# Kernel optimization log

Measured on AMD Instinct MI355X. Metric: run time of the kernel, lower is better.

Reference implementation:

```python
import jax, jax.numpy as jnp
import numpy as np

N_QUBITS = 12
BATCH = 2048
N_CLASSES = 10


def build_tape(n):
    # 2 layers of: RX on all wires (id 0), RY (id 1), RZ (id 2), then a CRX ring
    # (id 4 forward in layer 0, id 5 reversed in layer 1). 96 gates total for n=12.
    tape = []
    for layer in range(2):
        for i in range(n):
            tape.append(("rx", (i,)))
        for i in range(n):
            tape.append(("ry", (i,)))
        for i in range(n):
            tape.append(("rz", (i,)))
        order = range(n) if layer == 0 else range(n - 1, -1, -1)
        for i in order:
            tape.append(("crx", (i, (i + 1) % n)))
    return tape


def rx_mat(t):
    c = jnp.cos(t / 2).astype(jnp.complex64)
    s = jnp.sin(t / 2).astype(jnp.complex64)
    return jnp.stack([jnp.stack([c, -1j * s]), jnp.stack([-1j * s, c])])


def ry_mat(t):
    c = jnp.cos(t / 2).astype(jnp.complex64)
    s = jnp.sin(t / 2).astype(jnp.complex64)
    return jnp.stack([jnp.stack([c, -s]), jnp.stack([s, c])])


def rz_mat(t):
    em = jnp.exp(-1j * t.astype(jnp.complex64) / 2)
    ep = jnp.exp(1j * t.astype(jnp.complex64) / 2)
    z = jnp.zeros((), jnp.complex64)
    return jnp.stack([jnp.stack([em, z]), jnp.stack([z, ep])])


def apply_1q(psi, U, w):
    # psi: [B] + [2]*n, gate on wire w (axis 1+w)
    psi = jnp.moveaxis(psi, 1 + w, -1)
    psi = psi @ U.T
    return jnp.moveaxis(psi, -1, 1 + w)


def apply_crx(psi, theta, c, t):
    a_c, a_t = 1 + c, 1 + t
    psi = jnp.moveaxis(psi, a_c, 1)  # control -> axis 1
    if a_t < a_c:
        a_t += 1
    psi = jnp.moveaxis(psi, a_t, -1)  # target -> last axis
    U = rx_mat(theta)
    p1 = psi[:, 1] @ U.T  # apply RX only on control=1 branch
    psi = jnp.stack([psi[:, 0], p1], axis=1)
    psi = jnp.moveaxis(psi, -1, a_t)
    return jnp.moveaxis(psi, 1, a_c)


def expvals(psi, n):
    # <X_i>, <Y_i>, <Z_i> for each qubit; returns [B, 3n] ordered X..Y..Z (PL order)
    xs, ys, zs = [], [], []
    for i in range(n):
        p = jnp.moveaxis(psi, 1 + i, -1).reshape(psi.shape[0], -1, 2)
        z = jnp.sum(jnp.abs(p[..., 0]) ** 2 - jnp.abs(p[..., 1]) ** 2, axis=1)
        cross = jnp.sum(jnp.conj(p[..., 0]) * p[..., 1], axis=1)
        xs.append(2.0 * jnp.real(cross))
        ys.append(2.0 * jnp.imag(cross))
        zs.append(jnp.real(z))
    return jnp.stack(xs + ys + zs, axis=1).astype(jnp.float32)


def setup_inputs() -> dict:
    key = jax.random.key(0)
    k0, k1, k2 = jax.random.split(key, 3)
    sv = jax.random.normal(k0, (BATCH, 2 ** N_QUBITS), dtype=jnp.float32)
    sv = sv / jnp.linalg.norm(sv, axis=1, keepdims=True)  # valid quantum states
    n_gates = len(build_tape(N_QUBITS))
    angles = jax.random.normal(k1, (n_gates,), dtype=jnp.float32)
    W = jax.random.normal(k2, (N_CLASSES, 3 * N_QUBITS), dtype=jnp.float32) * 0.1
    b = jnp.zeros((N_CLASSES,), jnp.float32)
    return {"state_vectors": sv, "angles": angles, "W": W, "b": b}


def reference(state_vectors, angles, W, b):
    tape = build_tape(N_QUBITS)
    psi = state_vectors.astype(jnp.complex64).reshape((-1,) + (2,) * N_QUBITS)
    for g, (kind, wires) in enumerate(tape):
        th = angles[g]
        if kind == "rx":
            psi = apply_1q(psi, rx_mat(th), wires[0])
        elif kind == "ry":
            psi = apply_1q(psi, ry_mat(th), wires[0])
        elif kind == "rz":
            psi = apply_1q(psi, rz_mat(th), wires[0])
        else:
            psi = apply_crx(psi, th, wires[0], wires[1])
    feats = expvals(psi, N_QUBITS)  # [B, 3*n_qubits]
    return feats @ W.T + b
```

## Files before the change

kernel.cpp:

```cpp
#include <hip/hip_runtime.h>

#define DIM 4096
using F2 = float2;


__device__ __forceinline__ int swz(int i)            { return i ^ (i >> 6); }
__device__ __forceinline__ int addrA(int r, int t)   { return (r << 8) | t; }
__device__ __forceinline__ int addrB(int r, int t)   { return ((t >> 5) << 9) | (r << 5) | (t & 31); }
__device__ __forceinline__ int addrC(int r, int t)   { return ((t >> 2) << 6) | (r << 2) | (t & 3); }
__device__ __forceinline__ int addrD(int r, int t)   { return ((r >> 3) << 11) | (t << 3) | (r & 7); }

__device__ __forceinline__ F2 pk_mul_bl(F2 a, F2 u) {
    F2 d;
    asm("v_pk_mul_f32 %0, %1, %2 op_sel:[0,0] op_sel_hi:[1,0]"
        : "=v"(d) : "v"(a), "v"(u));
    return d;
}
__device__ __forceinline__ void pk_cross(F2& d, F2 a, F2 u) {
    asm("v_pk_fma_f32 %0, %1, %2, %0 op_sel:[1,1,0] op_sel_hi:[0,1,1] neg_lo:[1,0,0]"
        : "+v"(d) : "v"(a), "v"(u));
}
__device__ __forceinline__ void pk_fma_bl(F2& d, F2 a, F2 u) {
    asm("v_pk_fma_f32 %0, %1, %2, %0 op_sel:[0,0,0] op_sel_hi:[1,0,1]"
        : "+v"(d) : "v"(a), "v"(u));
}
__device__ __forceinline__ void pk_swapneg(F2& d, F2 a, F2 cs) {
    asm("v_pk_fma_f32 %0, %1, %2, %0 op_sel:[1,1,0] op_sel_hi:[0,1,1] neg_hi:[1,0,0]"
        : "+v"(d) : "v"(a), "v"(cs));
}
__device__ __forceinline__ void pk_fma(F2& d, F2 a, F2 b) {
    asm("v_pk_fma_f32 %0, %1, %2, %0" : "+v"(d) : "v"(a), "v"(b));
}
__device__ __forceinline__ void pk_imacc(F2& d, F2 a0, F2 a1) {
    asm("v_pk_fma_f32 %0, %1, %2, %0 op_sel:[0,1,0] op_sel_hi:[1,0,1] neg_hi:[1,0,0]"
        : "+v"(d) : "v"(a0), "v"(a1));
}
__device__ __forceinline__ F2 pk_cmul(F2 u, F2 a) {
    F2 d = pk_mul_bl(a, u);
    pk_cross(d, a, u);
    return d;
}
__device__ __forceinline__ void pk_cfma(F2& d, F2 u, F2 a) {
    pk_fma_bl(d, a, u);
    pk_cross(d, a, u);
}

__device__ __forceinline__ void build_u(float tx, float ty, float tz, float* u) {
    float sx = sinf(0.5f*tx), cx = cosf(0.5f*tx);
    float sy = sinf(0.5f*ty), cy = cosf(0.5f*ty);
    float sz = sinf(0.5f*tz), cz = cosf(0.5f*tz);
    float A00r = cy*cx, A00i =  sy*sx;
    float A01r = -sy*cx, A01i = -cy*sx;
    float A10r =  sy*cx, A10i = -cy*sx;
    float A11r =  cy*cx, A11i = -sy*sx;
    u[0] = cz*A00r + sz*A00i;  u[1] = cz*A00i - sz*A00r;
    u[2] = cz*A01r + sz*A01i;  u[3] = cz*A01i - sz*A01r;
    u[4] = cz*A10r - sz*A10i;  u[5] = cz*A10i + sz*A10r;
    u[6] = cz*A11r - sz*A11i;  u[7] = cz*A11i + sz*A11r;
}

__global__ void prep_kernel(const float* __restrict__ ang, float* __restrict__ coef) {
    int t = threadIdx.x;
    if (t < 24) {
        int l = t / 12, q = t % 12;
        float u[8];
        build_u(ang[48*l + q], ang[48*l + 12 + q], ang[48*l + 24 + q], u);
#pragma unroll
        for (int j = 0; j < 8; ++j) coef[t * 8 + j] = u[j];
    } else if (t < 48) {
        int g = t - 24;
        float th = 0.5f * ang[g < 12 ? 36 + g : 72 + g];
        coef[192 + g * 2]     = cosf(th);
        coef[192 + g * 2 + 1] = sinf(th);
    }
}

template<int M>
__device__ __forceinline__ void g1q(F2* amp, const float* __restrict__ u) {
    F2 u00 = {u[0], u[1]}, u01 = {u[2], u[3]};
    F2 u10 = {u[4], u[5]}, u11 = {u[6], u[7]};
#pragma unroll
    for (int r0 = 0; r0 < 16; ++r0) {
        if (r0 & M) continue;
        const int r1 = r0 + M;
        F2 a0 = amp[r0], a1 = amp[r1];
        F2 n0 = pk_cmul(u00, a0); pk_cfma(n0, u01, a1);
        F2 n1 = pk_cmul(u10, a0); pk_cfma(n1, u11, a1);
        amp[r0] = n0; amp[r1] = n1;
    }
}

template<int MC, int MT>
__device__ __forceinline__ void crx(F2* amp, F2 cs) {
#pragma unroll
    for (int r0 = 0; r0 < 16; ++r0) {
        if (!(r0 & MC) || (r0 & MT)) continue;
        const int r1 = r0 + MT;
        F2 a0 = amp[r0], a1 = amp[r1];
        F2 n0 = pk_mul_bl(a0, cs); pk_swapneg(n0, a1, cs);
        F2 n1 = pk_mul_bl(a1, cs); pk_swapneg(n1, a0, cs);
        amp[r0] = n0; amp[r1] = n1;
    }
}

template<int M>
__device__ __forceinline__ void expv(const F2* amp, int q, int lane,
                                     float& fx, float& fy, float& fz) {
    F2 zp = {0.f, 0.f}, zm = {0.f, 0.f}, xp = {0.f, 0.f}, ip = {0.f, 0.f};
#pragma unroll
    for (int r0 = 0; r0 < 16; ++r0) {
        if (r0 & M) continue;
        const int r1 = r0 + M;
        F2 a0 = amp[r0], a1 = amp[r1];
        pk_fma(zp, a0, a0);
        pk_fma(zm, a1, a1);
        pk_fma(xp, a0, a1);
        pk_imacc(ip, a0, a1);
    }
    float zz = (zp.x + zp.y) - (zm.x + zm.y);
    float xr = 2.f * (xp.x + xp.y);
    float xi = 2.f * (ip.x + ip.y);
#pragma unroll
    for (int off = 32; off; off >>= 1) {
        xr += __shfl_xor(xr, off);
        xi += __shfl_xor(xi, off);
        zz += __shfl_xor(zz, off);
    }
    if (lane == q) { fx = xr; fy = xi; fz = zz; }
}

#define XPOSE(CUR, NXT) \
  { _Pragma("unroll") for (int r = 0; r < 16; ++r) psi[swz(CUR(r, t))] = amp[r]; \
    __syncthreads(); \
    _Pragma("unroll") for (int r = 0; r < 16; ++r) amp[r] = psi[swz(NXT(r, t))]; \
    __syncthreads(); }

#define U0(q, M)        g1q<M>(amp, cf + (q) * 8)
#define U1(q, M)        g1q<M>(amp, cf + (12 + (q)) * 8)
#define CR0(c, MC, MT)  crx<MC, MT>(amp, F2{cf[192 + (c)*2], cf[192 + (c)*2 + 1]})
#define CR1(c, MC, MT)  crx<MC, MT>(amp, F2{cf[192 + (23-(c))*2], cf[192 + (23-(c))*2 + 1]})
#define EXPV(q, M)      expv<M>(amp, q, lane, fx, fy, fz)

__global__ __launch_bounds__(256, 1)
void qsim_kernel(const float* __restrict__ sv,
                 const float* __restrict__ cf,
                 const float* __restrict__ W,
                 const float* __restrict__ bvec,
                 float* __restrict__ out)
{
    __shared__ F2 psi[DIM];
    const int t = threadIdx.x;
    const int b = blockIdx.x;
    const int lane = t & 63, w = t >> 6;

    F2 amp[16];
    const float* svb = sv + (size_t)b * DIM;
#pragma unroll
    for (int r = 0; r < 16; ++r)
        amp[r] = make_float2(svb[(r << 8) | t], 0.f);

    float fx = 0.f, fy = 0.f, fz = 0.f;

    U0(0, 8); U0(1, 4); U0(2, 2); U0(3, 1);
    CR0(0, 8, 4); CR0(1, 4, 2); CR0(2, 2, 1);
    XPOSE(addrA, addrB);

    U0(4, 4); U0(5, 2); U0(6, 1);
    CR0(3, 8, 4); CR0(4, 4, 2); CR0(5, 2, 1);
    XPOSE(addrB, addrC);

    U0(7, 4); U0(8, 2); U0(9, 1);
    CR0(6, 8, 4); CR0(7, 4, 2); CR0(8, 2, 1);
    XPOSE(addrC, addrD);

    U0(10, 2); U0(11, 1);
    CR0(9, 4, 2); CR0(10, 2, 1); CR0(11, 1, 8);
    U1(9, 4); U1(10, 2); U1(11, 1); U1(0, 8);
    CR1(11, 1, 8); CR1(10, 2, 1); CR1(9, 4, 2);
    EXPV(10, 2); EXPV(11, 1);
    XPOSE(addrD, addrC);

    U1(6, 8); U1(7, 4); U1(8, 2);
    CR1(8, 2, 1); CR1(7, 4, 2); CR1(6, 8, 4);
    EXPV(9, 1); EXPV(8, 2); EXPV(7, 4);
    XPOSE(addrC, addrB);

    U1(3, 8); U1(4, 4); U1(5, 2);
    CR1(5, 2, 1); CR1(4, 4, 2); CR1(3, 8, 4);
    EXPV(6, 1); EXPV(5, 2); EXPV(4, 4);
    XPOSE(addrB, addrA);

    U1(1, 4); U1(2, 2);
    CR1(2, 2, 1); CR1(1, 4, 2); CR1(0, 8, 4);
    EXPV(0, 8); EXPV(1, 4); EXPV(2, 2); EXPV(3, 1);

    float* fbuf = (float*)psi;
    if (lane < 12) {
        fbuf[w * 36 + lane]      = fx;
        fbuf[w * 36 + 12 + lane] = fy;
        fbuf[w * 36 + 24 + lane] = fz;
    }
    __syncthreads();
    if (t < 10) {
        float a = bvec[t];
#pragma unroll
        for (int f = 0; f < 36; ++f)
            a += W[t * 36 + f] * (fbuf[f] + fbuf[36 + f] + fbuf[72 + f] + fbuf[108 + f]);
        out[(size_t)b * 10 + t] = a;
    }
}

extern "C" void kernel_launch(void* const* d_in, const int* in_sizes, int n_in,
                              void* d_out, int out_size, void* d_ws, size_t ws_size,
                              hipStream_t stream) {
    const float* sv     = (const float*)d_in[0];
    const float* angles = (const float*)d_in[1];
    const float* W      = (const float*)d_in[2];
    const float* bvec   = (const float*)d_in[3];
    float* out  = (float*)d_out;
    float* coef = (float*)d_ws;
    int batch = in_sizes[0] / DIM;
    prep_kernel<<<1, 64, 0, stream>>>(angles, coef);
    qsim_kernel<<<batch, 256, 0, stream>>>(sv, coef, W, bvec, out);
}
```

Measured before the change: 141.2 us.

## Hold 32 amplitudes per thread and fold CRX gates into single-qubit unitaries

Each block now runs 128 threads that each hold 32 amplitudes, which cuts the shared-memory transposes from six to four and brings in new XOR swizzles. The layer-0 CRX gates are folded into the following wire's fused single-qubit unitary on the host-side prep kernel, and a selector picks the plain or CRX-folded matrix by control bit. This removes a separate CRX pass in layer 0 and some barrier traffic. In exchange, register pressure roughly doubles and there are fewer waves to hide latency, and the CRX fold plus the new addressing must exactly match the gate order.

```diff
diff --git a/kernel.cpp b/kernel.cpp
--- a/kernel.cpp
+++ b/kernel.cpp
@@ -4,11 +4,11 @@
 using F2 = float2;
 
 
-__device__ __forceinline__ int swz(int i)            { return i ^ (i >> 6); }
-__device__ __forceinline__ int addrA(int r, int t)   { return (r << 8) | t; }
-__device__ __forceinline__ int addrB(int r, int t)   { return ((t >> 5) << 9) | (r << 5) | (t & 31); }
-__device__ __forceinline__ int addrC(int r, int t)   { return ((t >> 2) << 6) | (r << 2) | (t & 3); }
-__device__ __forceinline__ int addrD(int r, int t)   { return ((r >> 3) << 11) | (t << 3) | (r & 7); }
+__device__ __forceinline__ int addrA(int r, int t) { return (r << 7) | t; }
+__device__ __forceinline__ int addrB(int r, int t) { return ((t >> 3) << 8) | (r << 3) | (t & 7); }
+__device__ __forceinline__ int addrC(int r, int t) { return ((r & 1) << 11) | (t << 4) | (r >> 1); }
+__device__ __forceinline__ int swzAB(int a) { return a ^ ((a >> 5) & 8); }
+__device__ __forceinline__ int swzBC(int a) { return a ^ ((a >> 4) & 15) ^ ((a >> 5) & 8); }
 
 __device__ __forceinline__ F2 pk_mul_bl(F2 a, F2 u) {
     F2 d;
@@ -61,17 +61,41 @@
 
 __global__ void prep_kernel(const float* __restrict__ ang, float* __restrict__ coef) {
     int t = threadIdx.x;
-    if (t < 24) {
-        int l = t / 12, q = t % 12;
-        float u[8];
-        build_u(ang[48*l + q], ang[48*l + 12 + q], ang[48*l + 24 + q], u);
-#pragma unroll
-        for (int j = 0; j < 8; ++j) coef[t * 8 + j] = u[j];
-    } else if (t < 48) {
-        int g = t - 24;
-        float th = 0.5f * ang[g < 12 ? 36 + g : 72 + g];
-        coef[192 + g * 2]     = cosf(th);
-        coef[192 + g * 2 + 1] = sinf(th);
+    if (t < 12) {
+        float u[8]; build_u(ang[t], ang[12+t], ang[24+t], u);
+#pragma unroll
+        for (int j = 0; j < 8; ++j) coef[t*8 + j] = u[j];
+    } else if (t < 24) {
+        int q = t - 12;
+        float u[8]; build_u(ang[48+q], ang[60+q], ang[72+q], u);
+#pragma unroll
+        for (int j = 0; j < 8; ++j) coef[192 + q*8 + j] = u[j];
+    } else if (t < 36) {
+        int c = t - 24;
+        float th = 0.5f * ang[95 - c];
+        coef[296 + c*2]     = cosf(th);
+        coef[296 + c*2 + 1] = sinf(th);
+    } else if (t < 47) {
+        int q = t - 35;
+        float u[8]; build_u(ang[q], ang[12+q], ang[24+q], u);
+        float c = cosf(0.5f*ang[36+q-1]), s = sinf(0.5f*ang[36+q-1]);
+        float m[8];
+        m[0] = c*u[0] + s*u[5];  m[1] = c*u[1] - s*u[4];
+        m[2] = c*u[2] + s*u[7];  m[3] = c*u[3] - s*u[6];
+        m[4] = s*u[1] + c*u[4];  m[5] = -s*u[0] + c*u[5];
+        m[6] = s*u[3] + c*u[6];  m[7] = -s*u[2] + c*u[7];
+#pragma unroll
+        for (int j = 0; j < 8; ++j) coef[96 + q*8 + j] = m[j];
+    } else if (t == 47) {
+        float u[8]; build_u(ang[48], ang[60], ang[72], u);
+        float c = cosf(0.5f*ang[47]), s = sinf(0.5f*ang[47]);
+        float m[8];
+        m[0] = c*u[0] + s*u[3];  m[1] = c*u[1] - s*u[2];
+        m[2] = s*u[1] + c*u[2];  m[3] = -s*u[0] + c*u[3];
+        m[4] = c*u[4] + s*u[7];  m[5] = c*u[5] - s*u[6];
+        m[6] = s*u[5] + c*u[6];  m[7] = -s*u[4] + c*u[7];
+#pragma unroll
+        for (int j = 0; j < 8; ++j) coef[288 + j] = m[j];
     }
 }
 
@@ -80,7 +104,7 @@
     F2 u00 = {u[0], u[1]}, u01 = {u[2], u[3]};
     F2 u10 = {u[4], u[5]}, u11 = {u[6], u[7]};
 #pragma unroll
-    for (int r0 = 0; r0 < 16; ++r0) {
+    for (int r0 = 0; r0 < 32; ++r0) {
         if (r0 & M) continue;
         const int r1 = r0 + M;
         F2 a0 = amp[r0], a1 = amp[r1];
@@ -90,10 +114,29 @@
     }
 }
 
+template<int MSEL, int M>
+__device__ __forceinline__ void fg1q(F2* amp, const float* __restrict__ uA,
+                                     const float* __restrict__ uB) {
+    F2 a00 = {uA[0], uA[1]}, a01 = {uA[2], uA[3]}, a10 = {uA[4], uA[5]}, a11 = {uA[6], uA[7]};
+    F2 b00 = {uB[0], uB[1]}, b01 = {uB[2], uB[3]}, b10 = {uB[4], uB[5]}, b11 = {uB[6], uB[7]};
+#pragma unroll
+    for (int r0 = 0; r0 < 32; ++r0) {
+        if (r0 & M) continue;
+        const int r1 = r0 + M;
+        const bool sel = (r0 & MSEL) != 0;
+        F2 u00 = sel ? b00 : a00, u01 = sel ? b01 : a01;
+        F2 u10 = sel ? b10 : a10, u11 = sel ? b11 : a11;
+        F2 a0 = amp[r0], a1 = amp[r1];
+        F2 n0 = pk_cmul(u00, a0); pk_cfma(n0, u01, a1);
+        F2 n1 = pk_cmul(u10, a0); pk_cfma(n1, u11, a1);
+        amp[r0] = n0; amp[r1] = n1;
+    }
+}
+
 template<int MC, int MT>
 __device__ __forceinline__ void crx(F2* amp, F2 cs) {
 #pragma unroll
-    for (int r0 = 0; r0 < 16; ++r0) {
+    for (int r0 = 0; r0 < 32; ++r0) {
         if (!(r0 & MC) || (r0 & MT)) continue;
         const int r1 = r0 + MT;
         F2 a0 = amp[r0], a1 = amp[r1];
@@ -108,7 +151,7 @@
                                      float& fx, float& fy, float& fz) {
     F2 zp = {0.f, 0.f}, zm = {0.f, 0.f}, xp = {0.f, 0.f}, ip = {0.f, 0.f};
 #pragma unroll
-    for (int r0 = 0; r0 < 16; ++r0) {
+    for (int r0 = 0; r0 < 32; ++r0) {
         if (r0 & M) continue;
         const int r1 = r0 + M;
         F2 a0 = amp[r0], a1 = amp[r1];
@@ -129,19 +172,20 @@
     if (lane == q) { fx = xr; fy = xi; fz = zz; }
 }
 
-#define XPOSE(CUR, NXT) \
-  { _Pragma("unroll") for (int r = 0; r < 16; ++r) psi[swz(CUR(r, t))] = amp[r]; \
+#define XPOSE(CUR, NXT, SWZ) \
+  { _Pragma("unroll") for (int r = 0; r < 32; ++r) psi[SWZ(CUR(r, t))] = amp[r]; \
     __syncthreads(); \
-    _Pragma("unroll") for (int r = 0; r < 16; ++r) amp[r] = psi[swz(NXT(r, t))]; \
+    _Pragma("unroll") for (int r = 0; r < 32; ++r) amp[r] = psi[SWZ(NXT(r, t))]; \
     __syncthreads(); }
 
-#define U0(q, M)        g1q<M>(amp, cf + (q) * 8)
-#define U1(q, M)        g1q<M>(amp, cf + (12 + (q)) * 8)
-#define CR0(c, MC, MT)  crx<MC, MT>(amp, F2{cf[192 + (c)*2], cf[192 + (c)*2 + 1]})
-#define CR1(c, MC, MT)  crx<MC, MT>(amp, F2{cf[192 + (23-(c))*2], cf[192 + (23-(c))*2 + 1]})
-#define EXPV(q, M)      expv<M>(amp, q, lane, fx, fy, fz)
-
-__global__ __launch_bounds__(256, 1)
+#define U0P(q, M)        g1q<M>(amp, cf + (q)*8)
+#define FU0(q, MSEL, M)  fg1q<MSEL, M>(amp, cf + (q)*8, cf + 96 + (q)*8)
+#define U1P(q, M)        g1q<M>(amp, cf + 192 + (q)*8)
+#define FU1_0()          fg1q<2, 1>(amp, cf + 192, cf + 288)
+#define CR1(c, MC, MT)   crx<MC, MT>(amp, F2{cf[296 + (c)*2], cf[296 + (c)*2 + 1]})
+#define EXPV(q, M)       expv<M>(amp, q, lane, fx, fy, fz)
+
+__global__ __launch_bounds__(128, 1)
 void qsim_kernel(const float* __restrict__ sv,
                  const float* __restrict__ cf,
                  const float* __restrict__ W,
@@ -153,46 +197,36 @@
     const int b = blockIdx.x;
     const int lane = t & 63, w = t >> 6;
 
-    F2 amp[16];
+    F2 amp[32];
     const float* svb = sv + (size_t)b * DIM;
 #pragma unroll
-    for (int r = 0; r < 16; ++r)
-        amp[r] = make_float2(svb[(r << 8) | t], 0.f);
+    for (int r = 0; r < 32; ++r)
+        amp[r] = make_float2(svb[(r << 7) | t], 0.f);
 
     float fx = 0.f, fy = 0.f, fz = 0.f;
 
-    U0(0, 8); U0(1, 4); U0(2, 2); U0(3, 1);
-    CR0(0, 8, 4); CR0(1, 4, 2); CR0(2, 2, 1);
-    XPOSE(addrA, addrB);
-
-    U0(4, 4); U0(5, 2); U0(6, 1);
-    CR0(3, 8, 4); CR0(4, 4, 2); CR0(5, 2, 1);
-    XPOSE(addrB, addrC);
-
-    U0(7, 4); U0(8, 2); U0(9, 1);
-    CR0(6, 8, 4); CR0(7, 4, 2); CR0(8, 2, 1);
-    XPOSE(addrC, addrD);
-
-    U0(10, 2); U0(11, 1);
-    CR0(9, 4, 2); CR0(10, 2, 1); CR0(11, 1, 8);
-    U1(9, 4); U1(10, 2); U1(11, 1); U1(0, 8);
-    CR1(11, 1, 8); CR1(10, 2, 1); CR1(9, 4, 2);
-    EXPV(10, 2); EXPV(11, 1);
-    XPOSE(addrD, addrC);
-
-    U1(6, 8); U1(7, 4); U1(8, 2);
-    CR1(8, 2, 1); CR1(7, 4, 2); CR1(6, 8, 4);
-    EXPV(9, 1); EXPV(8, 2); EXPV(7, 4);
-    XPOSE(addrC, addrB);
-
-    U1(3, 8); U1(4, 4); U1(5, 2);
-    CR1(5, 2, 1); CR1(4, 4, 2); CR1(3, 8, 4);
-    EXPV(6, 1); EXPV(5, 2); EXPV(4, 4);
-    XPOSE(addrB, addrA);
-
-    U1(1, 4); U1(2, 2);
-    CR1(2, 2, 1); CR1(1, 4, 2); CR1(0, 8, 4);
-    EXPV(0, 8); EXPV(1, 4); EXPV(2, 2); EXPV(3, 1);
+    U0P(0, 16);
+    FU0(1, 16, 8); FU0(2, 8, 4); FU0(3, 4, 2); FU0(4, 2, 1);
+    XPOSE(addrA, addrB, swzAB);
+
+    FU0(5, 16, 8); FU0(6, 8, 4); FU0(7, 4, 2); FU0(8, 2, 1);
+    XPOSE(addrB, addrC, swzBC);
+
+    FU0(9, 16, 8); FU0(10, 8, 4); FU0(11, 4, 2);
+    FU1_0();
+    U1P(8, 16); U1P(9, 8); U1P(10, 4); U1P(11, 2);
+    CR1(11, 2, 1); CR1(10, 4, 2); CR1(9, 8, 4); CR1(8, 16, 8);
+    EXPV(9, 8); EXPV(10, 4); EXPV(11, 2);
+    XPOSE(addrC, addrB, swzBC);
+
+    U1P(4, 16); U1P(5, 8); U1P(6, 4); U1P(7, 2);
+    CR1(7, 2, 1); CR1(6, 4, 2); CR1(5, 8, 4); CR1(4, 16, 8);
+    EXPV(5, 8); EXPV(6, 4); EXPV(7, 2); EXPV(8, 1);
+    XPOSE(addrB, addrA, swzAB);
+
+    U1P(1, 8); U1P(2, 4); U1P(3, 2);
+    CR1(3, 2, 1); CR1(2, 4, 2); CR1(1, 8, 4); CR1(0, 16, 8);
+    EXPV(0, 16); EXPV(1, 8); EXPV(2, 4); EXPV(3, 2); EXPV(4, 1);
 
     float* fbuf = (float*)psi;
     if (lane < 12) {
@@ -205,7 +239,7 @@
         float a = bvec[t];
 #pragma unroll
         for (int f = 0; f < 36; ++f)
-            a += W[t * 36 + f] * (fbuf[f] + fbuf[36 + f] + fbuf[72 + f] + fbuf[108 + f]);
+            a += W[t * 36 + f] * (fbuf[f] + fbuf[36 + f]);
         out[(size_t)b * 10 + t] = a;
     }
 }
@@ -221,5 +255,5 @@
     float* coef = (float*)d_ws;
     int batch = in_sizes[0] / DIM;
     prep_kernel<<<1, 64, 0, stream>>>(angles, coef);
-    qsim_kernel<<<batch, 256, 0, stream>>>(sv, coef, W, bvec, out);
-}
+    qsim_kernel<<<batch, 128, 0, stream>>>(sv, coef, W, bvec, out);
+}
```

Measured after the change: 135.7 us. -3.9%, faster.
